# Kernel optimization log

Hardware: AMD Instinct MI355X
Metric: run time of the kernel (lower is better)

Reference implementation:

```python
import jax, jax.numpy as jnp
import numpy as np

ITERS = 10


def setup_inputs() -> dict:
    key = jax.random.key(0)
    k0, k1 = jax.random.split(key)
    B, D, H, W = 4, 64, 64, 64
    feat0 = jax.random.normal(k0, (B, D, H, W), dtype=jnp.float32)
    feat1 = jax.random.normal(k1, (B, D, H, W), dtype=jnp.float32)
    bin_score = jnp.asarray(1.0, dtype=jnp.float32)  # learned scalar parameter
    return {"feat0": feat0, "feat1": feat1, "bin_score": bin_score}


def _cdist(x, y):
    # torch.cdist(p=2): euclidean distance between rows. x: [b,m,d], y: [b,n,d]
    x2 = jnp.sum(x * x, axis=-1)[:, :, None]          # [b,m,1]
    y2 = jnp.sum(y * y, axis=-1)[:, None, :]          # [b,1,n]
    xy = jnp.einsum('bmd,bnd->bmn', x, y)             # [b,m,n]
    d2 = jnp.maximum(x2 + y2 - 2.0 * xy, 0.0)
    return jnp.sqrt(d2)


def _log_sinkhorn(Z, log_mu, log_nu, iters):
    # Z: [b, m+1, n+1]; log_mu: [b, m+1]; log_nu: [b, n+1]
    u0 = jnp.zeros_like(log_mu)
    v0 = jnp.zeros_like(log_nu)

    def body(i, uv):
        u, v = uv
        u = log_mu - jax.nn.logsumexp(Z + v[:, None, :], axis=2)
        v = log_nu - jax.nn.logsumexp(Z + u[:, :, None], axis=1)
        return (u, v)

    u, v = jax.lax.fori_loop(0, iters, body, (u0, v0))
    return Z + u[:, :, None] + v[:, None, :]


def _forward(feat0, feat1, bin_score):
    b, d, h, w = feat0.shape
    f0 = feat0.transpose(0, 2, 3, 1).reshape(b, h * w, d)
    f1 = feat1.transpose(0, 2, 3, 1).reshape(b, h * w, d)
    distance = _cdist(f0, f1)                         # [b, m, n]
    m, n = h * w, h * w
    dt = distance.dtype

    bins0 = jnp.broadcast_to(bin_score, (b, m, 1)).astype(dt)
    bins1 = jnp.broadcast_to(bin_score, (b, 1, n)).astype(dt)
    binsa = jnp.broadcast_to(bin_score, (b, 1, 1)).astype(dt)
    couplings = jnp.concatenate([
        jnp.concatenate([distance, bins0], axis=-1),
        jnp.concatenate([bins1, binsa], axis=-1),
    ], axis=1)                                        # [b, m+1, n+1]

    ms = jnp.asarray(m, dt)
    ns = jnp.asarray(n, dt)
    norm = -jnp.log(ms + ns)
    log_mu = jnp.concatenate([jnp.full((m,), norm, dtype=dt), (jnp.log(ns) + norm)[None]])
    log_nu = jnp.concatenate([jnp.full((n,), norm, dtype=dt), (jnp.log(ms) + norm)[None]])
    log_mu = jnp.broadcast_to(log_mu[None], (b, m + 1))
    log_nu = jnp.broadcast_to(log_nu[None], (b, n + 1))

    Z = _log_sinkhorn(couplings, log_mu, log_nu, ITERS)
    Z = Z - norm
    gamma = jnp.exp(Z)                                # [b, m+1, n+1]

    matching_loss = jnp.mean(jnp.sum(gamma[:, :-1, :-1] * distance, axis=2))
    dustbin_loss = jnp.mean(gamma[:, :, -1]) + jnp.mean(gamma[:, :-1, :])
    return matching_loss, dustbin_loss, gamma


def reference(feat0, feat1, bin_score):
    return _forward(feat0, feat1, bin_score)
```

## Files before the change

### kernel.cpp

```cpp
#include <hip/hip_runtime.h>
#include <math.h>

#define BB 4
#define DD 64
#define MM 4096
#define M1 4097
#define NORMC 9.0109133472792788f
#define CSH 11.0f
#define SCLX 1.0e12f
#define INVSCLX 1.0e-12f

typedef __attribute__((ext_vector_type(8))) short bf16x8;
typedef __attribute__((ext_vector_type(4))) float f32x4;

__device__ __forceinline__ f32x4 mfma16(bf16x8 a, bf16x8 b, f32x4 c) {
    return __builtin_amdgcn_mfma_f32_16x16x32_bf16(a, b, c, 0, 0, 0);
}
__device__ __forceinline__ unsigned short f2bf(float x) {
    unsigned u = __float_as_uint(x);
    u += 0x7fffu + ((u >> 16) & 1u);
    return (unsigned short)(u >> 16);
}

__global__ void __launch_bounds__(256)
prep_kernel(const float* __restrict__ f0, const float* __restrict__ f1,
            unsigned short* __restrict__ h0, unsigned short* __restrict__ h1) {
    __shared__ float T[64][65];
    const int b = blockIdx.y;
    const int p0 = blockIdx.x * 64;
    const float* src = (blockIdx.z == 0 ? f0 : f1) + (size_t)b * DD * MM;
    unsigned short* dh = (blockIdx.z == 0 ? h0 : h1) + (size_t)b * MM * DD;
    const int tid = threadIdx.x;
#pragma unroll
    for (int l = 0; l < 16; ++l) {
        int idx = l * 256 + tid;
        T[idx >> 6][idx & 63] = src[(idx >> 6) * MM + p0 + (idx & 63)];
    }
    __syncthreads();
    const int p = tid >> 2;
    const int cs = (tid & 3) * 16;
    unsigned hw[8];
#pragma unroll
    for (int k = 0; k < 8; ++k) {
        unsigned short a = f2bf(T[cs + 2 * k][p]);
        unsigned short c = f2bf(T[cs + 2 * k + 1][p]);
        hw[k] = (unsigned)a | ((unsigned)c << 16);
    }
    size_t base = (size_t)(p0 + p) * DD + cs;
    *(uint4*)(dh + base)     = make_uint4(hw[0], hw[1], hw[2], hw[3]);
    *(uint4*)(dh + base + 8) = make_uint4(hw[4], hw[5], hw[6], hw[7]);
}

__global__ void __launch_bounds__(256)
norms_kernel(const float* __restrict__ f0, const float* __restrict__ f1,
             float* __restrict__ n0, float* __restrict__ n1) {
    int t = blockIdx.x * 256 + threadIdx.x;
    if (t >= BB * MM) return;
    int b = t / MM, p = t % MM;
    const float* s0 = f0 + (size_t)b * DD * MM + p;
    const float* s1 = f1 + (size_t)b * DD * MM + p;
    float a = 0.f, c = 0.f;
#pragma unroll 8
    for (int k = 0; k < DD; ++k) {
        float x = s0[(size_t)k * MM]; a = fmaf(x, x, a);
        float y = s1[(size_t)k * MM]; c = fmaf(y, y, c);
    }
    n0[t] = a; n1[t] = c;
}

__global__ void __launch_bounds__(256)
distEB_kernel(const unsigned short* __restrict__ h0, const unsigned short* __restrict__ h1,
              const float* __restrict__ n0, const float* __restrict__ n1,
              uint2* __restrict__ EB) {
    __shared__ unsigned char sc[4][640];
    const int id = blockIdx.x;
    const int xcd = id & 7, slot = id >> 3;
    const int b = xcd >> 1;
    const int x = slot * 2 + (xcd & 1);
    const int r0 = x * 32;
    const int tid = threadIdx.x;
    const int w = tid >> 6, l = tid & 63, lg = l >> 4, lc = l & 15;
    const size_t fb = (size_t)b * MM * DD;

    bf16x8 Ah[2][2];
    float n0r[2][4];
#pragma unroll
    for (int st = 0; st < 2; ++st) {
        const unsigned short* pa = h0 + fb + (size_t)(r0 + st * 16 + lc) * DD + 8 * lg;
        Ah[st][0] = *(const bf16x8*)pa; Ah[st][1] = *(const bf16x8*)(pa + 32);
#pragma unroll
        for (int e = 0; e < 4; ++e)
            n0r[st][e] = n0[b * MM + r0 + st * 16 + 4 * lg + e];
    }

    for (int tt = 0; tt < 64; ++tt) {
        const int jt = w * 64 + tt;
        const int j0 = jt * 16;
        const unsigned short* pb = h1 + fb + (size_t)(j0 + lc) * DD + 8 * lg;
        bf16x8 Bh0 = *(const bf16x8*)pb, Bh1 = *(const bf16x8*)(pb + 32);
        float n1j = n1[b * MM + j0 + lc];
        unsigned pk[2];
#pragma unroll
        for (int st = 0; st < 2; ++st) {
            f32x4 acc = {0.f, 0.f, 0.f, 0.f};
            acc = mfma16(Ah[st][0], Bh0, acc);
            acc = mfma16(Ah[st][1], Bh1, acc);
            float Ev[4];
#pragma unroll
            for (int e = 0; e < 4; ++e) {
                float d2 = fmaxf(__builtin_fmaf(-2.f, acc[e], n0r[st][e] + n1j), 0.f);
                Ev[e] = __expf(sqrtf(d2) - CSH);
            }
            int p = __builtin_amdgcn_cvt_pk_fp8_f32(Ev[0], Ev[1], 0, false);
            p = __builtin_amdgcn_cvt_pk_fp8_f32(Ev[2], Ev[3], p, true);
            pk[st] = (unsigned)p;
        }
        *(unsigned*)&sc[w][lc * 40 + 4 * lg]      = pk[0];
        *(unsigned*)&sc[w][lc * 40 + 16 + 4 * lg] = pk[1];
        uint2 v = *(const uint2*)&sc[w][lc * 40 + 8 * lg];
        EB[(((size_t)(b * 128 + x)) * 256 + jt) * 64 + l] = v;
    }
}

__global__ void __launch_bounds__(512)
sinkF_kernel(const uint2* __restrict__ EB,
             const float* __restrict__ csPrev, float* __restrict__ csCur,
             const float* __restrict__ sxpPrev, float* __restrict__ sxpCur,
             const float* __restrict__ xmmPrev, float* __restrict__ xmmCur,
             float* __restrict__ X, const float* __restrict__ bin, int first) {
    __shared__ float Wl[4096];
    __shared__ float ps[256];
    __shared__ float XL[32];
    __shared__ float sh[8];
    __shared__ float shWMM;
    const int bid = blockIdx.x;
    const int b = bid >> 7, x = bid & 127;
    const int tid = threadIdx.x;
    const int w = tid >> 6, l = tid & 63, lg = l >> 4, lc = l & 15;
    const float bs = *bin;
    const float KC = __expf(-NORMC - CSH);
    const float EBt = __expf(bs - CSH);
    const float HB = 0.5f * __expf(-bs);

    if (first) {
#pragma unroll
        for (int k = 0; k < 8; ++k) Wl[k * 512 + tid] = 1.0f;
        if (tid == 0) shWMM = 1.0f;
        if (l == 0) sh[w] = 512.f * 8.f / 8.f;
    } else {
        const float xmmP = xmmPrev[b];
        if (tid < 64) {
            float s = sxpPrev[b * 128 + tid] + sxpPrev[b * 128 + 64 + tid];
#pragma unroll
            for (int off = 1; off < 64; off <<= 1) s += __shfl_xor(s, off);
            if (tid == 0) shWMM = HB / (s + xmmP);
        }
        const float db = EBt * xmmP;
        float local = 0.f;
#pragma unroll
        for (int k = 0; k < 8; ++k) {
            float cs = csPrev[b * MM + k * 512 + tid];
            float wv = KC / fmaf(cs, INVSCLX, db);
            Wl[k * 512 + tid] = wv;
            local += wv;
        }
#pragma unroll
        for (int off = 1; off < 64; off <<= 1) local += __shfl_xor(local, off);
        if (l == 0) sh[w] = local;
    }
    __syncthreads();
    const float wMMprev = shWMM;
    const float wmmRow = EBt * wMMprev;
    if (x == 0 && tid == 0) {
        float sumW = ((sh[0] + sh[1]) + (sh[2] + sh[3]))
                   + ((sh[4] + sh[5]) + (sh[6] + sh[7]));
        xmmCur[b] = HB / (sumW + wMMprev);
    }

    const uint2* EP = EB + (((size_t)(b * 128 + x)) * 256 + w * 32) * 64 + l;
    uint2 ec[32];
#pragma unroll
    for (int k = 0; k < 32; ++k) ec[k] = EP[(size_t)k * 64];

    float rs[8] = {};
#pragma unroll
    for (int k = 0; k < 32; ++k) {
        float wv = Wl[(w * 32 + k) * 16 + lc];
        auto p0 = __builtin_amdgcn_cvt_pk_f32_fp8((int)ec[k].x, false);
        auto p1 = __builtin_amdgcn_cvt_pk_f32_fp8((int)ec[k].x, true);
        auto p2 = __builtin_amdgcn_cvt_pk_f32_fp8((int)ec[k].y, false);
        auto p3 = __builtin_amdgcn_cvt_pk_f32_fp8((int)ec[k].y, true);
        rs[0] = fmaf(p0[0], wv, rs[0]); rs[1] = fmaf(p0[1], wv, rs[1]);
        rs[2] = fmaf(p1[0], wv, rs[2]); rs[3] = fmaf(p1[1], wv, rs[3]);
        rs[4] = fmaf(p2[0], wv, rs[4]); rs[5] = fmaf(p2[1], wv, rs[5]);
        rs[6] = fmaf(p3[0], wv, rs[6]); rs[7] = fmaf(p3[1], wv, rs[7]);
    }
#pragma unroll
    for (int off = 1; off < 16; off <<= 1)
#pragma unroll
        for (int t = 0; t < 8; ++t) rs[t] += __shfl_xor(rs[t], off);
    if (lc == 0) {
#pragma unroll
        for (int t = 0; t < 8; ++t) ps[w * 32 + 8 * lg + t] = rs[t];
    }
    __syncthreads();
    if (tid < 32) {
        float s = 0.f;
#pragma unroll
        for (int k = 0; k < 8; ++k) s += ps[k * 32 + tid];
        float xv = KC / (s + wmmRow);
        X[b * MM + x * 32 + tid] = xv;
        XL[tid] = xv * SCLX;
        float t = xv;
#pragma unroll
        for (int off = 1; off < 32; off <<= 1) t += __shfl_xor(t, off);
        if (tid == 0) sxpCur[b * 128 + x] = t;
    }
    __syncthreads();

    float f0 = XL[8 * lg + 0], f1 = XL[8 * lg + 1];
    float f2 = XL[8 * lg + 2], f3 = XL[8 * lg + 3];
    float f4 = XL[8 * lg + 4], f5 = XL[8 * lg + 5];
    float f6 = XL[8 * lg + 6], f7 = XL[8 * lg + 7];
    int u0 = __builtin_amdgcn_cvt_pk_fp8_f32(f0, f1, 0, false);
    u0 = __builtin_amdgcn_cvt_pk_fp8_f32(f2, f3, u0, true);
    int u1 = __builtin_amdgcn_cvt_pk_fp8_f32(f4, f5, 0, false);
    u1 = __builtin_amdgcn_cvt_pk_fp8_f32(f6, f7, u1, true);
    long long av = (long long)(((unsigned long long)(unsigned)u1 << 32) | (unsigned)u0);
    const f32x4 zero = {0.f, 0.f, 0.f, 0.f};
#pragma unroll
    for (int k = 0; k < 32; ++k) {
        long long bv = (long long)(((unsigned long long)ec[k].y << 32) | ec[k].x);
        f32x4 c = __builtin_amdgcn_mfma_f32_16x16x32_fp8_fp8(av, bv, zero, 0, 0, 0);
        if (l < 16) atomicAdd(&csCur[b * MM + (w * 32 + k) * 16 + l], c[0]);
    }
}

__global__ void __launch_bounds__(256)
finF_kernel(const uint2* __restrict__ EB, const float* __restrict__ X,
            const float* __restrict__ cs10, const float* __restrict__ sxp10,
            const float* __restrict__ xmm10, const float* __restrict__ bin,
            float* __restrict__ G, float* __restrict__ pA, float* __restrict__ pB) {
    const int bid = blockIdx.x;
    const int tid = threadIdx.x;
    const float bs = *bin;
    const float KC = __expf(-NORMC - CSH);
    const float EBt = __expf(bs - CSH);
    const float HB = 0.5f * __expf(-bs);
    if (bid >= BB * 128) {
        __shared__ float wmm10s[4];
        if (tid < 256) {
            int bb = tid >> 6, ll = tid & 63;
            float s = sxp10[bb * 128 + ll] + sxp10[bb * 128 + 64 + ll];
#pragma unroll
            for (int off = 1; off < 64; off <<= 1) s += __shfl_xor(s, off);
            if (ll == 0) wmm10s[bb] = HB / (s + xmm10[bb]);
        }
        __syncthreads();
        const int eb = bid - BB * 128;
        const float CC = __expf(NORMC + bs);
        int t = eb * 256 + tid;
        float pc = 0.f, pr = 0.f;
        if (t < BB * M1) {
            int b = t / M1, j = t % M1;
            float wj = (j < MM) ? KC / fmaf(cs10[b * MM + j], INVSCLX, EBt * xmm10[b])
                                : wmm10s[b];
            float g = CC * xmm10[b] * wj;
            G[((size_t)b * M1 + MM) * M1 + j] = g;
            if (j == MM) pc += g;
        } else if (t < BB * M1 + BB * MM) {
            int q = t - BB * M1;
            int b = q / MM, i = q % MM;
            float g = CC * X[b * MM + i] * wmm10s[b];
            G[((size_t)b * M1 + i) * M1 + MM] = g;
            pc += g; pr += g;
        }
#pragma unroll
        for (int off = 1; off < 64; off <<= 1) {
            pc += __shfl_xor(pc, off);
            pr += __shfl_xor(pr, off);
        }
        __shared__ float e0[4], e1[4];
        if ((tid & 63) == 0) { e0[tid >> 6] = pc; e1[tid >> 6] = pr; }
        __syncthreads();
        if (tid == 0) {
            pB[eb * 2 + 0] = e0[0] + e0[1] + e0[2] + e0[3];
            pB[eb * 2 + 1] = e1[0] + e1[1] + e1[2] + e1[3];
        }
        return;
    }
    __shared__ float T[256][36];
    __shared__ float Wl[4096];
    __shared__ float XL[32];
    const int b = bid >> 7, x = bid & 127;
    const int w = tid >> 6, l = tid & 63, lg = l >> 4, lc = l & 15;
    {
        const float db = EBt * xmm10[b];
#pragma unroll
        for (int k = 0; k < 16; ++k) {
            float cs = cs10[b * MM + k * 256 + tid];
            Wl[k * 256 + tid] = KC / fmaf(cs, INVSCLX, db);
        }
    }
    if (tid < 32) XL[tid] = X[b * MM + x * 32 + tid] * __expf(NORMC + CSH);
    __syncthreads();

    const uint2* EBb = EB + ((size_t)(b * 128 + x)) * 256 * 64;
    float pm = 0.f, pr = 0.f;
    for (int ch = 0; ch < 16; ++ch) {
#pragma unroll
        for (int q = 0; q < 4; ++q) {
            const int jt = ch * 16 + w * 4 + q;
            uint2 ev = EBb[(size_t)jt * 64 + l];
            float wv = Wl[jt * 16 + lc];
            auto p0 = __builtin_amdgcn_cvt_pk_f32_fp8((int)ev.x, false);
            auto p1 = __builtin_amdgcn_cvt_pk_f32_fp8((int)ev.x, true);
            auto p2 = __builtin_amdgcn_cvt_pk_f32_fp8((int)ev.y, false);
            auto p3 = __builtin_amdgcn_cvt_pk_f32_fp8((int)ev.y, true);
            float Ef[8] = {p0[0], p0[1], p1[0], p1[1], p2[0], p2[1], p3[0], p3[1]};
            float g[8];
#pragma unroll
            for (int t = 0; t < 8; ++t) {
                g[t] = Ef[t] * XL[8 * lg + t] * wv;
                pm = fmaf(g[t], (Ef[t] > 0.f) ? (CSH + __logf(Ef[t])) : 0.f, pm);
                pr += g[t];
            }
            const int jl = (w * 4 + q) * 16 + lc;
            f32x4 v0 = {g[0], g[1], g[2], g[3]};
            f32x4 v1 = {g[4], g[5], g[6], g[7]};
            *(f32x4*)&T[jl][8 * lg]     = v0;
            *(f32x4*)&T[jl][8 * lg + 4] = v1;
        }
        __syncthreads();
        float* gb = G + ((size_t)(b * M1 + x * 32)) * M1 + ch * 256 + tid;
#pragma unroll
        for (int r = 0; r < 32; ++r) gb[(size_t)r * M1] = T[tid][r];
        __syncthreads();
    }
#pragma unroll
    for (int off = 1; off < 64; off <<= 1) {
        pm += __shfl_xor(pm, off);
        pr += __shfl_xor(pr, off);
    }
    __shared__ float s0[4], s1[4];
    if (l == 0) { s0[w] = pm; s1[w] = pr; }
    __syncthreads();
    if (tid == 0) {
        pA[bid * 2 + 0] = s0[0] + s0[1] + s0[2] + s0[3];
        pA[bid * 2 + 1] = s1[0] + s1[1] + s1[2] + s1[3];
    }
}

__global__ void __launch_bounds__(256)
reduce_out_kernel(const float* __restrict__ pA, int nA,
                  const float* __restrict__ pB, int nB, float* __restrict__ out) {
    const int tid = threadIdx.x;
    float pm = 0.f, prA = 0.f, pc = 0.f, prB = 0.f;
    for (int r = tid; r < nA; r += 256) { pm += pA[2 * r]; prA += pA[2 * r + 1]; }
    for (int r = tid; r < nB; r += 256) { pc += pB[2 * r]; prB += pB[2 * r + 1]; }
#pragma unroll
    for (int off = 1; off < 64; off <<= 1) {
        pm += __shfl_xor(pm, off);
        prA += __shfl_xor(prA, off);
        pc += __shfl_xor(pc, off);
        prB += __shfl_xor(prB, off);
    }
    __shared__ float a0[4], a1[4], a2[4], a3[4];
    if ((tid & 63) == 0) {
        int w = tid >> 6;
        a0[w] = pm; a1[w] = prA; a2[w] = pc; a3[w] = prB;
    }
    __syncthreads();
    if (tid == 0) {
        float PM = a0[0] + a0[1] + a0[2] + a0[3];
        float PRA = a1[0] + a1[1] + a1[2] + a1[3];
        float PC = a2[0] + a2[1] + a2[2] + a2[3];
        float PRB = a3[0] + a3[1] + a3[2] + a3[3];
        out[0] = PM / (4.0f * 4096.0f);
        out[1] = PC / (4.0f * 4097.0f) + (PRA + PRB) / (4.0f * 4096.0f * 4097.0f);
    }
}

extern "C" void kernel_launch(void* const* d_in, const int* in_sizes, int n_in,
                              void* d_out, int out_size, void* d_ws, size_t ws_size,
                              hipStream_t stream) {
    const float* feat0 = (const float*)d_in[0];
    const float* feat1 = (const float*)d_in[1];
    const float* bin   = (const float*)d_in[2];
    float* out = (float*)d_out;
    float* G   = out + 2;
    float* ws  = (float*)d_ws;

    const size_t OF_X   = 0;
    const size_t OF_XMM = 16384;
    const size_t OF_SXP = 16448;
    const size_t OF_CS  = 22080;
    const size_t OF_PA  = 202304;
    const size_t OF_PB  = 203328;
    const size_t OF_N0  = 203616;
    const size_t OF_N1  = 220000;
    const size_t OF_BF  = 236384;
    const size_t OF_E8  = 1284960;

    float* X   = ws + OF_X;
    float* XMM = ws + OF_XMM;
    float* SXP = ws + OF_SXP;
    float* CS  = ws + OF_CS;
    float* pA  = ws + OF_PA;
    float* pB  = ws + OF_PB;
    float* n0  = ws + OF_N0;
    float* n1  = ws + OF_N1;
    unsigned short* h0 = (unsigned short*)(ws + OF_BF);
    unsigned short* h1 = h0 + 1048576;
    uint2* EB = (uint2*)(ws + OF_E8);

    hipMemsetAsync(CS, 0, 11 * 16384 * sizeof(float), stream);
    prep_kernel<<<dim3(64, BB, 2), 256, 0, stream>>>(feat0, feat1, h0, h1);
    norms_kernel<<<64, 256, 0, stream>>>(feat0, feat1, n0, n1);
    distEB_kernel<<<512, 256, 0, stream>>>(h0, h1, n0, n1, EB);
    for (int k = 1; k <= 10; ++k) {
        sinkF_kernel<<<512, 512, 0, stream>>>(
            EB,
            CS + (size_t)(k - 1) * 16384, CS + (size_t)k * 16384,
            SXP + (size_t)(k - 1) * 512,  SXP + (size_t)k * 512,
            XMM + (size_t)(k - 1) * 4,    XMM + (size_t)k * 4,
            X, bin, (k == 1) ? 1 : 0);
    }
    finF_kernel<<<BB * 128 + 129, 256, 0, stream>>>(
        EB, X, CS + 10 * 16384, SXP + 10 * 512, XMM + 10 * 4, bin, G, pA, pB);
    reduce_out_kernel<<<1, 256, 0, stream>>>(pA, BB * 128, pB, 129, out);
}
```

Before: 395.1 us.

## Replace atomic column sums with per-block partials and last-blocks reduction

Each Sinkhorn iteration now writes per-block column partial sums to a buffer instead of issuing global atomicAdds. The last 64 blocks to finish, detected with a ticket counter and a spin-wait, reduce those partials and precompute the column weights W and the scalar state for the next iteration. The norms computation is folded into the prep kernel, the memset is replaced by in-kernel initialization, and the final reduction is merged into the finalize kernel via a last-block pattern. This removes atomic contention and several launches, at the cost of a larger partial-sum buffer (512x4096 floats) and a grid-wide spin that depends on the earlier-finishing blocks freeing CUs for the late ones.

```diff
diff --git a/kernel.cpp b/kernel.cpp
--- a/kernel.cpp
+++ b/kernel.cpp
@@ -24,12 +24,16 @@
 
 __global__ void __launch_bounds__(256)
 prep_kernel(const float* __restrict__ f0, const float* __restrict__ f1,
-            unsigned short* __restrict__ h0, unsigned short* __restrict__ h1) {
+            unsigned short* __restrict__ h0, unsigned short* __restrict__ h1,
+            float* __restrict__ n0, float* __restrict__ n1,
+            float* __restrict__ SK0, unsigned* __restrict__ cnt) {
     __shared__ float T[64][65];
+    __shared__ float NB[4][64];
     const int b = blockIdx.y;
     const int p0 = blockIdx.x * 64;
-    const float* src = (blockIdx.z == 0 ? f0 : f1) + (size_t)b * DD * MM;
-    unsigned short* dh = (blockIdx.z == 0 ? h0 : h1) + (size_t)b * MM * DD;
+    const int z = blockIdx.z;
+    const float* src = (z == 0 ? f0 : f1) + (size_t)b * DD * MM;
+    unsigned short* dh = (z == 0 ? h0 : h1) + (size_t)b * MM * DD;
     const int tid = threadIdx.x;
 #pragma unroll
     for (int l = 0; l < 16; ++l) {
@@ -37,6 +41,16 @@
         T[idx >> 6][idx & 63] = src[(idx >> 6) * MM + p0 + (idx & 63)];
     }
     __syncthreads();
+    {
+        const int p = tid & 63, seg = tid >> 6;
+        float nn = 0.f;
+#pragma unroll
+        for (int c = 0; c < 16; ++c) {
+            float v = T[seg * 16 + c][p];
+            nn = fmaf(v, v, nn);
+        }
+        NB[seg][p] = nn;
+    }
     const int p = tid >> 2;
     const int cs = (tid & 3) * 16;
     unsigned hw[8];
@@ -46,26 +60,18 @@
         unsigned short c = f2bf(T[cs + 2 * k + 1][p]);
         hw[k] = (unsigned)a | ((unsigned)c << 16);
     }
+    __syncthreads();
+    if (tid < 64) {
+        float n = NB[0][tid] + NB[1][tid] + NB[2][tid] + NB[3][tid];
+        (z == 0 ? n0 : n1)[b * MM + p0 + tid] = n;
+    }
     size_t base = (size_t)(p0 + p) * DD + cs;
     *(uint4*)(dh + base)     = make_uint4(hw[0], hw[1], hw[2], hw[3]);
     *(uint4*)(dh + base + 8) = make_uint4(hw[4], hw[5], hw[6], hw[7]);
-}
-
-__global__ void __launch_bounds__(256)
-norms_kernel(const float* __restrict__ f0, const float* __restrict__ f1,
-             float* __restrict__ n0, float* __restrict__ n1) {
-    int t = blockIdx.x * 256 + threadIdx.x;
-    if (t >= BB * MM) return;
-    int b = t / MM, p = t % MM;
-    const float* s0 = f0 + (size_t)b * DD * MM + p;
-    const float* s1 = f1 + (size_t)b * DD * MM + p;
-    float a = 0.f, c = 0.f;
-#pragma unroll 8
-    for (int k = 0; k < DD; ++k) {
-        float x = s0[(size_t)k * MM]; a = fmaf(x, x, a);
-        float y = s1[(size_t)k * MM]; c = fmaf(y, y, c);
-    }
-    n0[t] = a; n1[t] = c;
+    if (blockIdx.x == 0 && b == 0 && z == 0) {
+        if (tid < 8) SK0[tid] = 1.0f;
+        if (tid >= 8 && tid < 24) cnt[tid - 8] = 0u;
+    }
 }
 
 __global__ void __launch_bounds__(256)
@@ -123,16 +129,17 @@
 }
 
 __global__ void __launch_bounds__(512)
-sinkF_kernel(const uint2* __restrict__ EB,
-             const float* __restrict__ csPrev, float* __restrict__ csCur,
-             const float* __restrict__ sxpPrev, float* __restrict__ sxpCur,
-             const float* __restrict__ xmmPrev, float* __restrict__ xmmCur,
-             float* __restrict__ X, const float* __restrict__ bin, int first) {
+sinkF2_kernel(const uint2* __restrict__ EB, float* __restrict__ W,
+              float* __restrict__ X, const float* __restrict__ SkP,
+              float* __restrict__ SkC, float* __restrict__ swp,
+              float* __restrict__ sxp, float* __restrict__ psum,
+              unsigned* __restrict__ cnt, const float* __restrict__ bin, int first) {
     __shared__ float Wl[4096];
     __shared__ float ps[256];
     __shared__ float XL[32];
-    __shared__ float sh[8];
-    __shared__ float shWMM;
+    __shared__ float CS2[2][256];
+    __shared__ float shS[2];
+    __shared__ unsigned shTick;
     const int bid = blockIdx.x;
     const int b = bid >> 7, x = bid & 127;
     const int tid = threadIdx.x;
@@ -141,41 +148,16 @@
     const float KC = __expf(-NORMC - CSH);
     const float EBt = __expf(bs - CSH);
     const float HB = 0.5f * __expf(-bs);
+    const float wMMp = first ? 1.0f : SkP[4 + b];
 
     if (first) {
 #pragma unroll
         for (int k = 0; k < 8; ++k) Wl[k * 512 + tid] = 1.0f;
-        if (tid == 0) shWMM = 1.0f;
-        if (l == 0) sh[w] = 512.f * 8.f / 8.f;
     } else {
-        const float xmmP = xmmPrev[b];
-        if (tid < 64) {
-            float s = sxpPrev[b * 128 + tid] + sxpPrev[b * 128 + 64 + tid];
-#pragma unroll
-            for (int off = 1; off < 64; off <<= 1) s += __shfl_xor(s, off);
-            if (tid == 0) shWMM = HB / (s + xmmP);
-        }
-        const float db = EBt * xmmP;
-        float local = 0.f;
-#pragma unroll
-        for (int k = 0; k < 8; ++k) {
-            float cs = csPrev[b * MM + k * 512 + tid];
-            float wv = KC / fmaf(cs, INVSCLX, db);
-            Wl[k * 512 + tid] = wv;
-            local += wv;
-        }
-#pragma unroll
-        for (int off = 1; off < 64; off <<= 1) local += __shfl_xor(local, off);
-        if (l == 0) sh[w] = local;
-    }
-    __syncthreads();
-    const float wMMprev = shWMM;
-    const float wmmRow = EBt * wMMprev;
-    if (x == 0 && tid == 0) {
-        float sumW = ((sh[0] + sh[1]) + (sh[2] + sh[3]))
-                   + ((sh[4] + sh[5]) + (sh[6] + sh[7]));
-        xmmCur[b] = HB / (sumW + wMMprev);
-    }
+#pragma unroll
+        for (int k = 0; k < 8; ++k) Wl[k * 512 + tid] = W[b * MM + k * 512 + tid];
+    }
+    __syncthreads();
 
     const uint2* EP = EB + (((size_t)(b * 128 + x)) * 256 + w * 32) * 64 + l;
     uint2 ec[32];
@@ -208,70 +190,122 @@
         float s = 0.f;
 #pragma unroll
         for (int k = 0; k < 8; ++k) s += ps[k * 32 + tid];
-        float xv = KC / (s + wmmRow);
+        float xv = KC / (s + EBt * wMMp);
         X[b * MM + x * 32 + tid] = xv;
         XL[tid] = xv * SCLX;
         float t = xv;
 #pragma unroll
         for (int off = 1; off < 32; off <<= 1) t += __shfl_xor(t, off);
-        if (tid == 0) sxpCur[b * 128 + x] = t;
-    }
-    __syncthreads();
-
-    float f0 = XL[8 * lg + 0], f1 = XL[8 * lg + 1];
-    float f2 = XL[8 * lg + 2], f3 = XL[8 * lg + 3];
-    float f4 = XL[8 * lg + 4], f5 = XL[8 * lg + 5];
-    float f6 = XL[8 * lg + 6], f7 = XL[8 * lg + 7];
-    int u0 = __builtin_amdgcn_cvt_pk_fp8_f32(f0, f1, 0, false);
-    u0 = __builtin_amdgcn_cvt_pk_fp8_f32(f2, f3, u0, true);
-    int u1 = __builtin_amdgcn_cvt_pk_fp8_f32(f4, f5, 0, false);
-    u1 = __builtin_amdgcn_cvt_pk_fp8_f32(f6, f7, u1, true);
-    long long av = (long long)(((unsigned long long)(unsigned)u1 << 32) | (unsigned)u0);
-    const f32x4 zero = {0.f, 0.f, 0.f, 0.f};
-#pragma unroll
-    for (int k = 0; k < 32; ++k) {
-        long long bv = (long long)(((unsigned long long)ec[k].y << 32) | ec[k].x);
-        f32x4 c = __builtin_amdgcn_mfma_f32_16x16x32_fp8_fp8(av, bv, zero, 0, 0, 0);
-        if (l < 16) atomicAdd(&csCur[b * MM + (w * 32 + k) * 16 + l], c[0]);
+        if (tid == 0) sxp[bid] = t;
+        float wv = Wl[x * 32 + tid];
+#pragma unroll
+        for (int off = 1; off < 32; off <<= 1) wv += __shfl_xor(wv, off);
+        if (tid == 0) swp[bid] = wv;
+    }
+    __syncthreads();
+
+    {
+        float f0 = XL[8 * lg + 0], f1 = XL[8 * lg + 1];
+        float f2 = XL[8 * lg + 2], f3 = XL[8 * lg + 3];
+        float f4 = XL[8 * lg + 4], f5 = XL[8 * lg + 5];
+        float f6 = XL[8 * lg + 6], f7 = XL[8 * lg + 7];
+        int u0 = __builtin_amdgcn_cvt_pk_fp8_f32(f0, f1, 0, false);
+        u0 = __builtin_amdgcn_cvt_pk_fp8_f32(f2, f3, u0, true);
+        int u1 = __builtin_amdgcn_cvt_pk_fp8_f32(f4, f5, 0, false);
+        u1 = __builtin_amdgcn_cvt_pk_fp8_f32(f6, f7, u1, true);
+        long long av = (long long)(((unsigned long long)(unsigned)u1 << 32) | (unsigned)u0);
+        float* po = psum + (size_t)bid * MM;
+        const f32x4 zero = {0.f, 0.f, 0.f, 0.f};
+#pragma unroll
+        for (int k = 0; k < 32; ++k) {
+            long long bv = (long long)(((unsigned long long)ec[k].y << 32) | ec[k].x);
+            f32x4 c = __builtin_amdgcn_mfma_f32_16x16x32_fp8_fp8(av, bv, zero, 0, 0, 0);
+            if (l < 16) po[(w * 32 + k) * 16 + l] = c[0];
+        }
+    }
+
+    __syncthreads();
+    __threadfence();
+    if (tid == 0) shTick = atomicAdd(cnt, 1u);
+    __syncthreads();
+    const unsigned tick = shTick;
+    if (tick < 448u) return;
+    if (tid == 0) {
+        while (__hip_atomic_load(cnt, __ATOMIC_ACQUIRE, __HIP_MEMORY_SCOPE_AGENT) < 512u)
+            __builtin_amdgcn_s_sleep(8);
+    }
+    __syncthreads();
+    __threadfence();
+
+    const int fb = (int)tick - 448;
+    const int fbb = fb >> 4;
+    const int slice = fb & 15;
+    const float wMMpF = first ? 1.0f : SkP[4 + fbb];
+    if (tid < 64) {
+        float s = swp[fbb * 128 + tid] + swp[fbb * 128 + 64 + tid];
+#pragma unroll
+        for (int off = 1; off < 64; off <<= 1) s += __shfl_xor(s, off);
+        if (tid == 0) shS[0] = HB / (s + wMMpF);
+    } else if (tid < 128) {
+        int t2 = tid - 64;
+        float s = sxp[fbb * 128 + t2] + sxp[fbb * 128 + 64 + t2];
+#pragma unroll
+        for (int off = 1; off < 64; off <<= 1) s += __shfl_xor(s, off);
+        if (t2 == 0) shS[1] = s;
+    }
+    __syncthreads();
+    const float xmmK = shS[0];
+    if (slice == 0 && tid == 0) {
+        SkC[fbb] = xmmK;
+        SkC[4 + fbb] = HB / (shS[1] + xmmK);
+    }
+    {
+        const int c = tid & 255;
+        const int h = tid >> 8;
+        const float* pp = psum + ((size_t)(fbb * 128 + h * 64)) * MM + slice * 256 + c;
+        float s = 0.f;
+#pragma unroll 8
+        for (int q = 0; q < 64; ++q) s += pp[(size_t)q * MM];
+        CS2[h][c] = s;
+    }
+    __syncthreads();
+    if (tid < 256) {
+        float t2 = CS2[0][tid] + CS2[1][tid];
+        W[fbb * MM + slice * 256 + tid] = KC / fmaf(t2, INVSCLX, EBt * xmmK);
     }
 }
 
 __global__ void __launch_bounds__(256)
-finF_kernel(const uint2* __restrict__ EB, const float* __restrict__ X,
-            const float* __restrict__ cs10, const float* __restrict__ sxp10,
-            const float* __restrict__ xmm10, const float* __restrict__ bin,
-            float* __restrict__ G, float* __restrict__ pA, float* __restrict__ pB) {
+finEB2_kernel(const uint2* __restrict__ EB, const float* __restrict__ X,
+              const float* __restrict__ W, const float* __restrict__ S,
+              const float* __restrict__ bin, float* __restrict__ G,
+              float* __restrict__ pA, float* __restrict__ pB,
+              unsigned* __restrict__ cnt, float* __restrict__ out) {
+    __shared__ float T[256][36];
+    __shared__ float Wl[4096];
+    __shared__ float XL[32];
+    __shared__ float a0[4], a1[4], a2[4], a3[4];
+    __shared__ unsigned tk;
     const int bid = blockIdx.x;
     const int tid = threadIdx.x;
+    const int w = tid >> 6, l = tid & 63, lg = l >> 4, lc = l & 15;
     const float bs = *bin;
-    const float KC = __expf(-NORMC - CSH);
-    const float EBt = __expf(bs - CSH);
-    const float HB = 0.5f * __expf(-bs);
+
     if (bid >= BB * 128) {
-        __shared__ float wmm10s[4];
-        if (tid < 256) {
-            int bb = tid >> 6, ll = tid & 63;
-            float s = sxp10[bb * 128 + ll] + sxp10[bb * 128 + 64 + ll];
-#pragma unroll
-            for (int off = 1; off < 64; off <<= 1) s += __shfl_xor(s, off);
-            if (ll == 0) wmm10s[bb] = HB / (s + xmm10[bb]);
-        }
-        __syncthreads();
         const int eb = bid - BB * 128;
         const float CC = __expf(NORMC + bs);
         int t = eb * 256 + tid;
         float pc = 0.f, pr = 0.f;
         if (t < BB * M1) {
             int b = t / M1, j = t % M1;
-            float wj = (j < MM) ? KC / fmaf(cs10[b * MM + j], INVSCLX, EBt * xmm10[b])
-                                : wmm10s[b];
-            float g = CC * xmm10[b] * wj;
+            float wj = (j < MM) ? W[b * MM + j] : S[4 + b];
+            float g = CC * S[b] * wj;
             G[((size_t)b * M1 + MM) * M1 + j] = g;
             if (j == MM) pc += g;
         } else if (t < BB * M1 + BB * MM) {
             int q = t - BB * M1;
             int b = q / MM, i = q % MM;
-            float g = CC * X[b * MM + i] * wmm10s[b];
+            float g = CC * X[b * MM + i] * S[4 + b];
             G[((size_t)b * M1 + i) * M1 + MM] = g;
             pc += g; pr += g;
         }
@@ -280,84 +314,73 @@
             pc += __shfl_xor(pc, off);
             pr += __shfl_xor(pr, off);
         }
-        __shared__ float e0[4], e1[4];
-        if ((tid & 63) == 0) { e0[tid >> 6] = pc; e1[tid >> 6] = pr; }
+        if (l == 0) { a0[w] = pc; a1[w] = pr; }
         __syncthreads();
         if (tid == 0) {
-            pB[eb * 2 + 0] = e0[0] + e0[1] + e0[2] + e0[3];
-            pB[eb * 2 + 1] = e1[0] + e1[1] + e1[2] + e1[3];
-        }
-        return;
-    }
-    __shared__ float T[256][36];
-    __shared__ float Wl[4096];
-    __shared__ float XL[32];
-    const int b = bid >> 7, x = bid & 127;
-    const int w = tid >> 6, l = tid & 63, lg = l >> 4, lc = l & 15;
-    {
-        const float db = EBt * xmm10[b];
-#pragma unroll
-        for (int k = 0; k < 16; ++k) {
-            float cs = cs10[b * MM + k * 256 + tid];
-            Wl[k * 256 + tid] = KC / fmaf(cs, INVSCLX, db);
-        }
-    }
-    if (tid < 32) XL[tid] = X[b * MM + x * 32 + tid] * __expf(NORMC + CSH);
-    __syncthreads();
-
-    const uint2* EBb = EB + ((size_t)(b * 128 + x)) * 256 * 64;
-    float pm = 0.f, pr = 0.f;
-    for (int ch = 0; ch < 16; ++ch) {
-#pragma unroll
-        for (int q = 0; q < 4; ++q) {
-            const int jt = ch * 16 + w * 4 + q;
-            uint2 ev = EBb[(size_t)jt * 64 + l];
-            float wv = Wl[jt * 16 + lc];
-            auto p0 = __builtin_amdgcn_cvt_pk_f32_fp8((int)ev.x, false);
-            auto p1 = __builtin_amdgcn_cvt_pk_f32_fp8((int)ev.x, true);
-            auto p2 = __builtin_amdgcn_cvt_pk_f32_fp8((int)ev.y, false);
-            auto p3 = __builtin_amdgcn_cvt_pk_f32_fp8((int)ev.y, true);
-            float Ef[8] = {p0[0], p0[1], p1[0], p1[1], p2[0], p2[1], p3[0], p3[1]};
-            float g[8];
-#pragma unroll
-            for (int t = 0; t < 8; ++t) {
-                g[t] = Ef[t] * XL[8 * lg + t] * wv;
-                pm = fmaf(g[t], (Ef[t] > 0.f) ? (CSH + __logf(Ef[t])) : 0.f, pm);
-                pr += g[t];
+            pB[eb * 2 + 0] = a0[0] + a0[1] + a0[2] + a0[3];
+            pB[eb * 2 + 1] = a1[0] + a1[1] + a1[2] + a1[3];
+        }
+    } else {
+        const int b = bid >> 7, x = bid & 127;
+#pragma unroll
+        for (int k = 0; k < 16; ++k) Wl[k * 256 + tid] = W[b * MM + k * 256 + tid];
+        if (tid < 32) XL[tid] = X[b * MM + x * 32 + tid] * __expf(NORMC + CSH);
+        __syncthreads();
+
+        const uint2* EBb = EB + ((size_t)(b * 128 + x)) * 256 * 64;
+        float pm = 0.f, pr = 0.f;
+        for (int ch = 0; ch < 16; ++ch) {
+#pragma unroll
+            for (int q = 0; q < 4; ++q) {
+                const int jt = ch * 16 + w * 4 + q;
+                uint2 ev = EBb[(size_t)jt * 64 + l];
+                float wv = Wl[jt * 16 + lc];
+                auto p0 = __builtin_amdgcn_cvt_pk_f32_fp8((int)ev.x, false);
+                auto p1 = __builtin_amdgcn_cvt_pk_f32_fp8((int)ev.x, true);
+                auto p2 = __builtin_amdgcn_cvt_pk_f32_fp8((int)ev.y, false);
+                auto p3 = __builtin_amdgcn_cvt_pk_f32_fp8((int)ev.y, true);
+                float Ef[8] = {p0[0], p0[1], p1[0], p1[1], p2[0], p2[1], p3[0], p3[1]};
+                float g[8];
+#pragma unroll
+                for (int t = 0; t < 8; ++t) {
+                    g[t] = Ef[t] * XL[8 * lg + t] * wv;
+                    pm = fmaf(g[t], (Ef[t] > 0.f) ? (CSH + __logf(Ef[t])) : 0.f, pm);
+                    pr += g[t];
+                }
+                const int jl = (w * 4 + q) * 16 + lc;
+                f32x4 v0 = {g[0], g[1], g[2], g[3]};
+                f32x4 v1 = {g[4], g[5], g[6], g[7]};
+                *(f32x4*)&T[jl][8 * lg]     = v0;
+                *(f32x4*)&T[jl][8 * lg + 4] = v1;
             }
-            const int jl = (w * 4 + q) * 16 + lc;
-            f32x4 v0 = {g[0], g[1], g[2], g[3]};
-            f32x4 v1 = {g[4], g[5], g[6], g[7]};
-            *(f32x4*)&T[jl][8 * lg]     = v0;
-            *(f32x4*)&T[jl][8 * lg + 4] = v1;
-        }
+            __syncthreads();
+            float* gb = G + ((size_t)(b * M1 + x * 32)) * M1 + ch * 256 + tid;
+#pragma unroll
+            for (int r = 0; r < 32; ++r) gb[(size_t)r * M1] = T[tid][r];
+            __syncthreads();
+        }
+#pragma unroll
+        for (int off = 1; off < 64; off <<= 1) {
+            pm += __shfl_xor(pm, off);
+            pr += __shfl_xor(pr, off);
+        }
+        if (l == 0) { a0[w] = pm; a1[w] = pr; }
         __syncthreads();
-        float* gb = G + ((size_t)(b * M1 + x * 32)) * M1 + ch * 256 + tid;
-#pragma unroll
-        for (int r = 0; r < 32; ++r) gb[(size_t)r * M1] = T[tid][r];
-        __syncthreads();
-    }
-#pragma unroll
-    for (int off = 1; off < 64; off <<= 1) {
-        pm += __shfl_xor(pm, off);
-        pr += __shfl_xor(pr, off);
-    }
-    __shared__ float s0[4], s1[4];
-    if (l == 0) { s0[w] = pm; s1[w] = pr; }
-    __syncthreads();
-    if (tid == 0) {
-        pA[bid * 2 + 0] = s0[0] + s0[1] + s0[2] + s0[3];
-        pA[bid * 2 + 1] = s1[0] + s1[1] + s1[2] + s1[3];
-    }
-}
-
-__global__ void __launch_bounds__(256)
-reduce_out_kernel(const float* __restrict__ pA, int nA,
-                  const float* __restrict__ pB, int nB, float* __restrict__ out) {
-    const int tid = threadIdx.x;
+        if (tid == 0) {
+            pA[bid * 2 + 0] = a0[0] + a0[1] + a0[2] + a0[3];
+            pA[bid * 2 + 1] = a1[0] + a1[1] + a1[2] + a1[3];
+        }
+    }
+
+    __syncthreads();
+    __threadfence();
+    if (tid == 0) tk = atomicAdd(cnt, 1u);
+    __syncthreads();
+    if (tk != (unsigned)(BB * 128 + 129 - 1)) return;
+    __threadfence();
     float pm = 0.f, prA = 0.f, pc = 0.f, prB = 0.f;
-    for (int r = tid; r < nA; r += 256) { pm += pA[2 * r]; prA += pA[2 * r + 1]; }
-    for (int r = tid; r < nB; r += 256) { pc += pB[2 * r]; prB += pB[2 * r + 1]; }
+    for (int r = tid; r < BB * 128; r += 256) { pm += pA[2 * r]; prA += pA[2 * r + 1]; }
+    for (int r = tid; r < 129; r += 256)      { pc += pB[2 * r]; prB += pB[2 * r + 1]; }
 #pragma unroll
     for (int off = 1; off < 64; off <<= 1) {
         pm += __shfl_xor(pm, off);
@@ -365,11 +388,8 @@
         pc += __shfl_xor(pc, off);
         prB += __shfl_xor(prB, off);
     }
-    __shared__ float a0[4], a1[4], a2[4], a3[4];
-    if ((tid & 63) == 0) {
-        int w = tid >> 6;
-        a0[w] = pm; a1[w] = prA; a2[w] = pc; a3[w] = prB;
-    }
+    __syncthreads();
+    if (l == 0) { a0[w] = pm; a1[w] = prA; a2[w] = pc; a3[w] = prB; }
     __syncthreads();
     if (tid == 0) {
         float PM = a0[0] + a0[1] + a0[2] + a0[3];
@@ -392,41 +412,41 @@
     float* ws  = (float*)d_ws;
 
     const size_t OF_X   = 0;
-    const size_t OF_XMM = 16384;
-    const size_t OF_SXP = 16448;
-    const size_t OF_CS  = 22080;
-    const size_t OF_PA  = 202304;
-    const size_t OF_PB  = 203328;
-    const size_t OF_N0  = 203616;
-    const size_t OF_N1  = 220000;
-    const size_t OF_BF  = 236384;
-    const size_t OF_E8  = 1284960;
+    const size_t OF_W   = 16384;
+    const size_t OF_SK  = 32768;
+    const size_t OF_SWP = 32864;
+    const size_t OF_SXP = 33376;
+    const size_t OF_CNT = 33888;
+    const size_t OF_PA  = 33904;
+    const size_t OF_PB  = 34928;
+    const size_t OF_N0  = 35200;
+    const size_t OF_N1  = 51584;
+    const size_t OF_PS  = 67968;
+    const size_t OF_BF  = 2165120;
+    const size_t OF_E8  = 3213696;
 
     float* X   = ws + OF_X;
-    float* XMM = ws + OF_XMM;
+    float* W   = ws + OF_W;
+    float* SK  = ws + OF_SK;
+    float* SWP = ws + OF_SWP;
     float* SXP = ws + OF_SXP;
-    float* CS  = ws + OF_CS;
+    unsigned* CNT = (unsigned*)(ws + OF_CNT);
     float* pA  = ws + OF_PA;
     float* pB  = ws + OF_PB;
     float* n0  = ws + OF_N0;
     float* n1  = ws + OF_N1;
+    float* PS  = ws + OF_PS;
     unsigned short* h0 = (unsigned short*)(ws + OF_BF);
     unsigned short* h1 = h0 + 1048576;
     uint2* EB = (uint2*)(ws + OF_E8);
 
-    hipMemsetAsync(CS, 0, 11 * 16384 * sizeof(float), stream);
-    prep_kernel<<<dim3(64, BB, 2), 256, 0, stream>>>(feat0, feat1, h0, h1);
-    norms_kernel<<<64, 256, 0, stream>>>(feat0, feat1, n0, n1);
+    prep_kernel<<<dim3(64, BB, 2), 256, 0, stream>>>(feat0, feat1, h0, h1, n0, n1, SK, CNT);
     distEB_kernel<<<512, 256, 0, stream>>>(h0, h1, n0, n1, EB);
     for (int k = 1; k <= 10; ++k) {
-        sinkF_kernel<<<512, 512, 0, stream>>>(
-            EB,
-            CS + (size_t)(k - 1) * 16384, CS + (size_t)k * 16384,
-            SXP + (size_t)(k - 1) * 512,  SXP + (size_t)k * 512,
-            XMM + (size_t)(k - 1) * 4,    XMM + (size_t)k * 4,
-            X, bin, (k == 1) ? 1 : 0);
-    }
-    finF_kernel<<<BB * 128 + 129, 256, 0, stream>>>(
-        EB, X, CS + 10 * 16384, SXP + 10 * 512, XMM + 10 * 4, bin, G, pA, pB);
-    reduce_out_kernel<<<1, 256, 0, stream>>>(pA, BB * 128, pB, 129, out);
-}
+        sinkF2_kernel<<<512, 512, 0, stream>>>(
+            EB, W, X, SK + (size_t)(k - 1) * 8, SK + (size_t)k * 8,
+            SWP, SXP, PS, CNT + (k - 1), bin, (k == 1) ? 1 : 0);
+    }
+    finEB2_kernel<<<BB * 128 + 129, 256, 0, stream>>>(
+        EB, X, W, SK + 80, bin, G, pA, pB, CNT + 10, out);
+}
```

Result: slower. 1.487 ms (+276.4%).
